# Optimization experiments

Measured on AMD Instinct MI355X. Metric: run time of the kernel, lower is better.

## Reference

```python
import jax, jax.numpy as jnp
import numpy as np

N_NODES = 100000
N_REL = 8
IN_DIM = 64
HID = 128
OUT = 64
N_EDGES = 640000


def setup_inputs() -> dict:
    key = jax.random.key(0)
    ks = jax.random.split(key, 24)

    def w(k, shape, fan_in):
        return jax.random.normal(k, shape, jnp.float32) / np.sqrt(fan_in).astype(np.float32)

    inp = {}
    inp["emb"] = jax.random.normal(ks[0], (N_NODES, IN_DIM), jnp.float32)
    dims = [(IN_DIM, HID), (HID, HID), (HID, HID // 2), (HID // 2, OUT)]
    for i, (di, do) in enumerate(dims, 1):
        inp[f"W{i}"] = w(ks[3 * i], (N_REL, di, do), di)      # per-relation weight
        inp[f"R{i}"] = w(ks[3 * i + 1], (di, do), di)          # root weight
        inp[f"B{i}"] = jnp.zeros((do,), jnp.float32)           # bias
    inp["g1"] = jnp.ones((HID,), jnp.float32)
    inp["b1"] = jnp.zeros((HID,), jnp.float32)
    inp["g2"] = jnp.ones((HID,), jnp.float32)
    inp["b2"] = jnp.zeros((HID,), jnp.float32)
    inp["ei"] = jax.random.randint(ks[20], (2, N_EDGES), 0, N_NODES, jnp.int32)
    inp["et"] = jax.random.randint(ks[21], (N_EDGES,), 0, N_REL, jnp.int32)
    return inp


def rgcn(x, ei, et, W, Wr, b):
    # PyG RGCNConv (aggr='mean'): out_i = x_i @ Wroot + b + sum_r mean_{j in N_r(i)} x_j @ W_r
    # Aggregate-then-transform: mean x[src] per (dst, rel) bin, then per-relation GEMM.
    n, r, d = x.shape[0], W.shape[0], x.shape[1]
    src, dst = ei[0], ei[1]
    seg = dst * r + et                                   # combined (node, relation) segment id
    agg = jax.ops.segment_sum(x[src], seg, num_segments=n * r)          # [N*R, d]
    cnt = jax.ops.segment_sum(jnp.ones((src.shape[0],), x.dtype), seg, num_segments=n * r)
    agg = (agg / jnp.maximum(cnt, 1.0)[:, None]).reshape(n, r, d)       # mean per relation
    return jnp.einsum('nri,rio->no', agg, W) + x @ Wr + b


def layer_norm(x, g, b, eps=1e-5):
    mu = jnp.mean(x, axis=-1, keepdims=True)
    var = jnp.mean((x - mu) ** 2, axis=-1, keepdims=True)
    return (x - mu) * jax.lax.rsqrt(var + eps) * g + b


def reference(emb, W1, R1, B1, W2, R2, B2, W3, R3, B3, W4, R4, B4, g1, b1, g2, b2, ei, et):
    # dropout is eval-mode identity
    x = jax.nn.relu(rgcn(emb, ei, et, W1, R1, B1))
    x = layer_norm(x, g1, b1)
    identity = x
    x = jax.nn.relu(rgcn(x, ei, et, W2, R2, B2))
    x = layer_norm(x + identity, g2, b2)
    x = jax.nn.relu(rgcn(x, ei, et, W3, R3, B3))
    return rgcn(x, ei, et, W4, R4, B4)
```

## Files before the change

kernel.cpp:

```cpp
#include <hip/hip_runtime.h>
#include <math.h>

#define NN 100000
#define NR 8
#define NE 640000
#define SEGN (NN * NR)
#define SPB 2048
#define NSB ((SEGN + SPB - 1) / SPB)

#define TILES 1563
#define HT1 782
#define HT2 781
#define HP1 (HT1 * 64)
#define HP2 (HT2 * 64)
#define HPF (TILES * 64)

typedef __attribute__((ext_vector_type(8))) __bf16 bf16x8;
typedef __attribute__((ext_vector_type(4))) float  f32x4;

__device__ __forceinline__ float bf2f(unsigned short b) {
    return __uint_as_float((unsigned)b << 16);
}
__device__ __forceinline__ unsigned short f2bf(float v) {
    __bf16 b = (__bf16)v;
    return __builtin_bit_cast(unsigned short, b);
}


__global__ __launch_bounds__(256) void count_kernel(
    const int* __restrict__ dst, const int* __restrict__ et, unsigned* __restrict__ cnt) {
    int e = blockIdx.x * 256 + threadIdx.x;
    if (e < NE) atomicAdd(&cnt[(size_t)et[e] * NN + dst[e]], 1u);
}

__global__ __launch_bounds__(256) void scan1_kernel(
    const unsigned* __restrict__ cnt, unsigned* __restrict__ bsum) {
    __shared__ unsigned red[256];
    int b = blockIdx.x, t = threadIdx.x;
    int i0 = b * SPB;
    unsigned s = 0;
#pragma unroll
    for (int k = 0; k < SPB / 256; ++k) {
        int i = i0 + k * 256 + t;
        if (i < SEGN) s += cnt[i];
    }
    red[t] = s;
    __syncthreads();
    for (int off = 128; off >= 1; off >>= 1) {
        if (t < off) red[t] += red[t + off];
        __syncthreads();
    }
    if (t == 0) bsum[b] = red[0];
}

__global__ __launch_bounds__(512) void scan2_kernel(
    unsigned* __restrict__ bsum, int* __restrict__ segoff) {
    __shared__ unsigned buf[512];
    int t = threadIdx.x;
    unsigned v = (t < NSB) ? bsum[t] : 0u;
    buf[t] = v;
    __syncthreads();
    for (int off = 1; off < 512; off <<= 1) {
        unsigned w = (t >= off) ? buf[t - off] : 0u;
        __syncthreads();
        buf[t] += w;
        __syncthreads();
    }
    if (t < NSB) bsum[t] = buf[t] - v;
    if (t == 0) segoff[SEGN] = NE;
}

__global__ __launch_bounds__(256) void scan3_kernel(
    const unsigned* __restrict__ cnt, const unsigned* __restrict__ bsum,
    int* __restrict__ segoff) {
    __shared__ unsigned lc[SPB];
    __shared__ unsigned tsum[256];
    int b = blockIdx.x, t = threadIdx.x;
    int i0 = b * SPB;
#pragma unroll
    for (int k = 0; k < SPB / 256; ++k) {
        int i = i0 + k * 256 + t;
        lc[k * 256 + t] = (i < SEGN) ? cnt[i] : 0u;
    }
    __syncthreads();
    unsigned s = 0;
#pragma unroll
    for (int k = 0; k < 8; ++k) s += lc[t * 8 + k];
    tsum[t] = s;
    __syncthreads();
    for (int off = 1; off < 256; off <<= 1) {
        unsigned w = (t >= off) ? tsum[t - off] : 0u;
        __syncthreads();
        tsum[t] += w;
        __syncthreads();
    }
    unsigned base = bsum[b] + tsum[t] - s;
#pragma unroll
    for (int k = 0; k < 8; ++k) {
        unsigned c = lc[t * 8 + k];
        lc[t * 8 + k] = base;
        base += c;
    }
    __syncthreads();
#pragma unroll
    for (int k = 0; k < SPB / 256; ++k) {
        int i = i0 + k * 256 + t;
        if (i < SEGN) segoff[i] = (int)lc[k * 256 + t];
    }
}

__global__ __launch_bounds__(256) void fill_kernel(
    const int* __restrict__ src, const int* __restrict__ dst, const int* __restrict__ et,
    const int* __restrict__ segoff, unsigned* __restrict__ cursor, int* __restrict__ esrc) {
    int e = blockIdx.x * 256 + threadIdx.x;
    if (e >= NE) return;
    int d = dst[e];
    int seg = et[e] * NN + d;
    int pos = segoff[seg] + (int)atomicAdd(&cursor[seg], 1u);
    esrc[pos] = src[e] | ((d & 3) << 17);
}

__global__ __launch_bounds__(256) void conv_emb(
    const float* __restrict__ emb, ushort* __restrict__ embb) {
    int i = blockIdx.x * 256 + threadIdx.x;
    if (i * 4 >= NN * 64) return;
    f32x4 v = *(const f32x4*)(emb + (size_t)i * 4);
    ushort4 o;
    o.x = f2bf(v[0]); o.y = f2bf(v[1]); o.z = f2bf(v[2]); o.w = f2bf(v[3]);
    *(ushort4*)(embb + (size_t)i * 4) = o;
}


template <int D, int O>
__global__ __launch_bounds__(256) void pack_kernel(
    const float* __restrict__ W, const float* __restrict__ Wr, __bf16* __restrict__ Wp) {
    constexpr int KT = D / 32, NTN = O / 16;
    int idx = blockIdx.x * 256 + threadIdx.x;
    if (idx >= (NR + 1) * KT * NTN * 64) return;
    int l = idx & 63;
    int rest = idx >> 6;
    int nt = rest % NTN; rest /= NTN;
    int kt = rest % KT;
    int r  = rest / KT;
    const float* srcw = (r < NR) ? (W + (size_t)r * D * O) : Wr;
    int n  = nt * 16 + (l & 15);
    int k0 = kt * 32 + (l >> 4) * 8;
    bf16x8 v;
#pragma unroll
    for (int j = 0; j < 8; ++j) {
        int p  = k0 + j;
        int kd = (D == 128) ? ((p >> 1) + ((p & 1) << 6)) : p;
        v[j] = (__bf16)srcw[(size_t)kd * O + n];
    }
    *(bf16x8*)(Wp + (size_t)idx * 8) = v;
}


template <int D, int XF>
__global__ __launch_bounds__(256) void gather_kernel(
    const void* __restrict__ xin, const int* __restrict__ segoff,
    const int* __restrict__ esrc, ushort* __restrict__ agg,
    int nbase, int agg_off, int HP)
{
    int wv = threadIdx.x >> 6, ln = threadIdx.x & 63;
    int r  = blockIdx.y;
    int i0 = blockIdx.x * 16 + wv * 4;
    int n0 = nbase + i0;

    const ushort*   xb = (const ushort*)xin;
    const unsigned* xs = (const unsigned*)xin;

    float ax[4] = {0, 0, 0, 0}, ay[4] = {0, 0, 0, 0};
    int eo[5];
#pragma unroll
    for (int k = 0; k <= 4; ++k) {
        int node = n0 + k; if (node > NN) node = NN;
        eo[k] = segoff[r * NN + node];
    }
    for (int ei = eo[0]; ei < eo[4]; ei += 4) {
        int nb = eo[4] - ei; if (nb > 4) nb = 4;
        int mm[4]; float vx[4], vy[4];
#pragma unroll
        for (int b = 0; b < 4; ++b) mm[b] = (b < nb) ? esrc[ei + b] : 0;
#pragma unroll
        for (int b = 0; b < 4; ++b) {
            if (b < nb) {
                int s = mm[b] & 0x1FFFF;
                if constexpr (XF == 1) {
                    unsigned w = xs[(size_t)s * 64 + ln];
                    vx[b] = bf2f((unsigned short)(w & 0xFFFFu));
                    vy[b] = bf2f((unsigned short)(w >> 16));
                } else {
                    vx[b] = bf2f(xb[(size_t)s * 64 + ln]);
                }
            }
        }
#pragma unroll
        for (int b = 0; b < 4; ++b) {
            if (b < nb) {
                int k = mm[b] >> 17;
#pragma unroll
                for (int kk = 0; kk < 4; ++kk) {
                    ax[kk] += (kk == k) ? vx[b] : 0.0f;
                    if constexpr (D == 128) ay[kk] += (kk == k) ? vy[b] : 0.0f;
                }
            }
        }
    }
#pragma unroll
    for (int k = 0; k < 4; ++k) {
        int c = eo[k + 1] - eo[k];
        float sc = (c > 0) ? 1.0f / (float)c : 0.0f;
        size_t row = ((size_t)r * HP + agg_off + i0 + k) * D;
        if constexpr (D == 128) {
            unsigned st = (unsigned)f2bf(ax[k] * sc) | ((unsigned)f2bf(ay[k] * sc) << 16);
            *((unsigned*)(agg + row) + ln) = st;
        } else {
            agg[row + ln] = f2bf(ax[k] * sc);
        }
    }
}


template <int D, int O, int MODE, int XF, int OF>
__global__ __launch_bounds__(256) void gemm_layer(
    const ushort* __restrict__ agg, const __bf16* __restrict__ Wp,
    const float* __restrict__ bias, const float* __restrict__ gamma,
    const float* __restrict__ beta, const unsigned* __restrict__ xres,
    const void* __restrict__ xroot, void* __restrict__ outv, int base, int HP)
{
    constexpr int KT = D / 32, NTN = O / 16;
    constexpr int PD = (D == 64) ? 8 : 3;
    int tid = threadIdx.x;
    int wv = tid >> 6, ln = tid & 63, lg = ln >> 4, lm = ln & 15;
    int i0 = blockIdx.x * 64 + wv * 16;

    const ushort* abase = agg + ((size_t)(i0 + lm)) * D + lg * 8;

    bf16x8 Aall[NR][KT];
#pragma unroll
    for (int r = 0; r < PD; ++r) {
        const ushort* ar = abase + (size_t)r * HP * D;
#pragma unroll
        for (int kt = 0; kt < KT; ++kt)
            Aall[r][kt] = *(const bf16x8*)(ar + kt * 32);
    }

    bf16x8 Aroot[KT];
    {
        int nrow = base + i0 + lm;
        if (nrow >= NN) nrow = NN - 1;
#pragma unroll
        for (int kt = 0; kt < KT; ++kt) {
            if constexpr (XF == 1) {
                Aroot[kt] = *(const bf16x8*)((const ushort*)xroot +
                                             (size_t)nrow * 128 + kt * 32 + lg * 8);
            } else {
                Aroot[kt] = *(const bf16x8*)((const ushort*)xroot +
                                             (size_t)nrow * 64 + kt * 32 + lg * 8);
            }
        }
    }

    f32x4 acc[NTN];
#pragma unroll
    for (int nt = 0; nt < NTN; ++nt)
#pragma unroll
        for (int q = 0; q < 4; ++q) acc[nt][q] = 0.0f;

#pragma unroll
    for (int r = 0; r < NR; ++r) {
        if (r + PD < NR) {
            const ushort* an = abase + (size_t)(r + PD) * HP * D;
#pragma unroll
            for (int kt = 0; kt < KT; ++kt)
                Aall[r + PD][kt] = *(const bf16x8*)(an + kt * 32);
        }
        const __bf16* bp = Wp + (((size_t)(r * KT) * NTN) << 9) + (ln << 3);
#pragma unroll
        for (int kt = 0; kt < KT; ++kt) {
            const __bf16* bpk = bp + (((size_t)(kt * NTN)) << 9);
#pragma unroll
            for (int nt = 0; nt < NTN; ++nt) {
                bf16x8 B = *(const bf16x8*)(bpk + ((size_t)nt << 9));
                acc[nt] = __builtin_amdgcn_mfma_f32_16x16x32_bf16(Aall[r][kt], B, acc[nt], 0, 0, 0);
            }
        }
    }
    {
        const __bf16* bp = Wp + (((size_t)(8 * KT) * NTN) << 9) + (ln << 3);
#pragma unroll
        for (int kt = 0; kt < KT; ++kt) {
            const __bf16* bpk = bp + (((size_t)(kt * NTN)) << 9);
#pragma unroll
            for (int nt = 0; nt < NTN; ++nt) {
                bf16x8 B = *(const bf16x8*)(bpk + ((size_t)nt << 9));
                acc[nt] = __builtin_amdgcn_mfma_f32_16x16x32_bf16(Aroot[kt], B, acc[nt], 0, 0, 0);
            }
        }
    }

    float bb[NTN], gg[NTN], be[NTN];
#pragma unroll
    for (int nt = 0; nt < NTN; ++nt) {
        bb[nt] = bias[nt * 16 + lm];
        if constexpr (MODE <= 1) {
            gg[nt] = gamma[nt * 16 + lm];
            be[nt] = beta[nt * 16 + lm];
        } else {
            gg[nt] = 0.0f; be[nt] = 0.0f;
        }
    }
#pragma unroll
    for (int q = 0; q < 4; ++q) {
        int row = lg * 4 + q;
        int n = base + i0 + row;
        int nc = (n < NN) ? n : 0;
        float v[NTN];
#pragma unroll
        for (int nt = 0; nt < NTN; ++nt) {
            v[nt] = acc[nt][q] + bb[nt];
            if constexpr (MODE <= 2) v[nt] = fmaxf(v[nt], 0.0f);
            if constexpr (MODE == 1) {
                unsigned w = xres[(size_t)nc * 64 + (nt & 3) * 16 + lm];
                v[nt] += bf2f((unsigned short)((nt < 4) ? (w & 0xFFFFu) : (w >> 16)));
            }
        }
        if constexpr (MODE <= 1) {
            float s1 = 0.0f, s2 = 0.0f;
#pragma unroll
            for (int nt = 0; nt < NTN; ++nt) { s1 += v[nt]; s2 += v[nt] * v[nt]; }
#pragma unroll
            for (int off = 1; off < 16; off <<= 1) {
                s1 += __shfl_xor(s1, off, 64);
                s2 += __shfl_xor(s2, off, 64);
            }
            float mu  = s1 * (1.0f / O);
            float var = s2 * (1.0f / O) - mu * mu;
            float rs  = rsqrtf(var + 1e-5f);
#pragma unroll
            for (int nt = 0; nt < NTN; ++nt) v[nt] = (v[nt] - mu) * rs * gg[nt] + be[nt];
        }
        if (n < NN) {
            if constexpr (OF == 0) {
#pragma unroll
                for (int nt = 0; nt < NTN; ++nt)
                    __builtin_nontemporal_store(
                        v[nt], (float*)outv + (size_t)n * O + nt * 16 + lm);
            } else if constexpr (OF == 1) {
#pragma unroll
                for (int nt = 0; nt < 4; ++nt)
                    ((unsigned*)outv)[(size_t)n * 64 + nt * 16 + lm] =
                        (unsigned)f2bf(v[nt]) | ((unsigned)f2bf(v[nt + 4]) << 16);
            } else {
#pragma unroll
                for (int nt = 0; nt < NTN; ++nt)
                    ((ushort*)outv)[(size_t)n * 64 + nt * 16 + lm] = f2bf(v[nt]);
            }
        }
    }
}


extern "C" void kernel_launch(void* const* d_in, const int* in_sizes, int n_in,
                              void* d_out, int out_size, void* d_ws, size_t ws_size,
                              hipStream_t stream) {
    const float* emb = (const float*)d_in[0];
    const float* W1  = (const float*)d_in[1];
    const float* R1  = (const float*)d_in[2];
    const float* B1  = (const float*)d_in[3];
    const float* W2  = (const float*)d_in[4];
    const float* R2  = (const float*)d_in[5];
    const float* B2  = (const float*)d_in[6];
    const float* W3  = (const float*)d_in[7];
    const float* R3  = (const float*)d_in[8];
    const float* B3  = (const float*)d_in[9];
    const float* W4  = (const float*)d_in[10];
    const float* R4  = (const float*)d_in[11];
    const float* B4  = (const float*)d_in[12];
    const float* g1  = (const float*)d_in[13];
    const float* b1  = (const float*)d_in[14];
    const float* g2  = (const float*)d_in[15];
    const float* b2  = (const float*)d_in[16];
    const int*   ei  = (const int*)d_in[17];
    const int*   et  = (const int*)d_in[18];
    const int* srcp = ei;
    const int* dstp = ei + NE;

    char* ws = (char*)d_ws;
    if (ws_size < 185721872u) return;
    int*      segoff = (int*)(ws + 0);
    int*      esrc   = (int*)(ws + 3200016);
    __bf16*   Wp1    = (__bf16*)(ws + 5760016);
    __bf16*   Wp2    = (__bf16*)(ws + 5907472);
    __bf16*   Wp3    = (__bf16*)(ws + 6202384);
    __bf16*   Wp4    = (__bf16*)(ws + 6349840);
    ushort*   embb   = (ushort*)(ws + 6423568);
    void*     x1     = (void*)(ws + 19223568);
    void*     x2     = (void*)(ws + 44823568);
    void*     x3     = (void*)(ws + 70423568);
    ushort*   agg    = (ushort*)(ws + 83223568);
    unsigned* cnt    = (unsigned*)(ws + 83223568);
    unsigned* cursor = (unsigned*)(ws + 86423568);
    unsigned* bsum   = (unsigned*)(ws + 89623568);
    float*    outp   = (float*)d_out;

    hipMemsetAsync(cnt, 0, 3200000, stream);
    hipMemsetAsync(cursor, 0, 3200000, stream);

    count_kernel<<<(NE + 255) / 256, 256, 0, stream>>>(dstp, et, cnt);
    scan1_kernel<<<NSB, 256, 0, stream>>>(cnt, bsum);
    scan2_kernel<<<1, 512, 0, stream>>>(bsum, segoff);
    scan3_kernel<<<NSB, 256, 0, stream>>>(cnt, bsum, segoff);
    fill_kernel<<<(NE + 255) / 256, 256, 0, stream>>>(
        srcp, dstp, et, segoff, cursor, esrc);
    conv_emb<<<(NN * 64 / 4 + 255) / 256, 256, 0, stream>>>(emb, embb);

    pack_kernel<64, 128><<<(9 * 2 * 8 * 64 + 255) / 256, 256, 0, stream>>>(W1, R1, Wp1);
    pack_kernel<128, 128><<<(9 * 4 * 8 * 64 + 255) / 256, 256, 0, stream>>>(W2, R2, Wp2);
    pack_kernel<128, 64><<<(9 * 4 * 4 * 64 + 255) / 256, 256, 0, stream>>>(W3, R3, Wp3);
    pack_kernel<64, 64><<<(9 * 2 * 4 * 64 + 255) / 256, 256, 0, stream>>>(W4, R4, Wp4);

    gather_kernel<64, 2><<<dim3(HP1 / 16, 8), 256, 0, stream>>>(embb, segoff, esrc, agg, 0, 0, HPF);
    gather_kernel<64, 2><<<dim3(HP2 / 16, 8), 256, 0, stream>>>(embb, segoff, esrc, agg, HP1, HP1, HPF);
    gemm_layer<64, 128, 0, 2, 1><<<HPF / 64, 256, 0, stream>>>(
        agg, Wp1, B1, g1, b1, nullptr, embb, x1, 0, HPF);

    gather_kernel<128, 1><<<dim3(25024 / 16, 8), 256, 0, stream>>>(x1, segoff, esrc, agg, 0, 0, HP1);
    gather_kernel<128, 1><<<dim3(25024 / 16, 8), 256, 0, stream>>>(x1, segoff, esrc, agg, 25024, 25024, HP1);
    gemm_layer<128, 128, 1, 1, 1><<<HP1 / 64, 256, 0, stream>>>(
        agg, Wp2, B2, g2, b2, (const unsigned*)x1, x1, x2, 0, HP1);
    gather_kernel<128, 1><<<dim3(25024 / 16, 8), 256, 0, stream>>>(x1, segoff, esrc, agg, HP1, 0, HP2);
    gather_kernel<128, 1><<<dim3(24960 / 16, 8), 256, 0, stream>>>(x1, segoff, esrc, agg, HP1 + 25024, 25024, HP2);
    gemm_layer<128, 128, 1, 1, 1><<<HP2 / 64, 256, 0, stream>>>(
        agg, Wp2, B2, g2, b2, (const unsigned*)x1, x1, x2, HP1, HP2);

    gather_kernel<128, 1><<<dim3(25024 / 16, 8), 256, 0, stream>>>(x2, segoff, esrc, agg, 0, 0, HP1);
    gather_kernel<128, 1><<<dim3(25024 / 16, 8), 256, 0, stream>>>(x2, segoff, esrc, agg, 25024, 25024, HP1);
    gemm_layer<128, 64, 2, 1, 2><<<HP1 / 64, 256, 0, stream>>>(
        agg, Wp3, B3, nullptr, nullptr, nullptr, x2, x3, 0, HP1);
    gather_kernel<128, 1><<<dim3(25024 / 16, 8), 256, 0, stream>>>(x2, segoff, esrc, agg, HP1, 0, HP2);
    gather_kernel<128, 1><<<dim3(24960 / 16, 8), 256, 0, stream>>>(x2, segoff, esrc, agg, HP1 + 25024, 25024, HP2);
    gemm_layer<128, 64, 2, 1, 2><<<HP2 / 64, 256, 0, stream>>>(
        agg, Wp3, B3, nullptr, nullptr, nullptr, x2, x3, HP1, HP2);

    gather_kernel<64, 2><<<dim3(HP1 / 16, 8), 256, 0, stream>>>(x3, segoff, esrc, agg, 0, 0, HPF);
    gather_kernel<64, 2><<<dim3(HP2 / 16, 8), 256, 0, stream>>>(x3, segoff, esrc, agg, HP1, HP1, HPF);
    gemm_layer<64, 64, 3, 2, 0><<<HPF / 64, 256, 0, stream>>>(
        agg, Wp4, B4, nullptr, nullptr, nullptr, x3, outp, 0, HPF);
}
```

Before: 741.2 us.

## Stage per-relation aggregate tiles through LDS with async global_load_lds double buffering

The GEMM kernel now copies each relation's 64-row aggregate tile into a double-buffered LDS array with global_load_lds, instead of prefetching many relation tiles into registers. The aggregation kernel writes rows with an XOR swizzle so that the LDS reads avoid bank conflicts. The aim is to cut register pressure, which raises occupancy, and to overlap the next relation's load with the current MFMAs. In exchange it adds a __syncthreads per relation and allocates up to 32KB of LDS per block.

```diff
diff --git a/kernel.cpp b/kernel.cpp
--- a/kernel.cpp
+++ b/kernel.cpp
@@ -24,6 +24,12 @@
 __device__ __forceinline__ unsigned short f2bf(float v) {
     __bf16 b = (__bf16)v;
     return __builtin_bit_cast(unsigned short, b);
+}
+
+__device__ __forceinline__ void gload16(const ushort* g, ushort* l) {
+    __builtin_amdgcn_global_load_lds(
+        (const __attribute__((address_space(1))) void*)g,
+        (__attribute__((address_space(3))) void*)l, 16, 0, 0);
 }
 
 
@@ -211,12 +217,13 @@
     for (int k = 0; k < 4; ++k) {
         int c = eo[k + 1] - eo[k];
         float sc = (c > 0) ? 1.0f / (float)c : 0.0f;
-        size_t row = ((size_t)r * HP + agg_off + i0 + k) * D;
+        int rw = agg_off + i0 + k;
+        size_t row = ((size_t)r * HP + rw) * D;
         if constexpr (D == 128) {
             unsigned st = (unsigned)f2bf(ax[k] * sc) | ((unsigned)f2bf(ay[k] * sc) << 16);
-            *((unsigned*)(agg + row) + ln) = st;
+            *((unsigned*)(agg + row) + (ln ^ ((rw & 7) << 2))) = st;
         } else {
-            agg[row + ln] = f2bf(ax[k] * sc);
+            agg[row + (ln ^ ((rw & 7) << 3))] = f2bf(ax[k] * sc);
         }
     }
 }
@@ -230,25 +237,28 @@
     const void* __restrict__ xroot, void* __restrict__ outv, int base, int HP)
 {
     constexpr int KT = D / 32, NTN = O / 16;
-    constexpr int PD = (D == 64) ? 8 : 3;
+    constexpr int NISS = (64 * D * 2) / (4 * 64 * 16);
+    __shared__ __align__(16) ushort sA[2][64 * D];
+
     int tid = threadIdx.x;
     int wv = tid >> 6, ln = tid & 63, lg = ln >> 4, lm = ln & 15;
-    int i0 = blockIdx.x * 64 + wv * 16;
-
-    const ushort* abase = agg + ((size_t)(i0 + lm)) * D + lg * 8;
-
-    bf16x8 Aall[NR][KT];
-#pragma unroll
-    for (int r = 0; r < PD; ++r) {
-        const ushort* ar = abase + (size_t)r * HP * D;
-#pragma unroll
-        for (int kt = 0; kt < KT; ++kt)
-            Aall[r][kt] = *(const bf16x8*)(ar + kt * 32);
-    }
+    int i0 = blockIdx.x * 64;
+
+    auto stage = [&](int r, int b) {
+        const ushort* src = agg + ((size_t)r * HP + i0) * D;
+        ushort* dst = &sA[b][0];
+#pragma unroll
+        for (int j = 0; j < NISS; ++j) {
+            int off_u = wv * (NISS * 512) + j * 512 + ln * 8;
+            gload16(src + off_u, dst + off_u);
+        }
+    };
+
+    stage(0, 0);
 
     bf16x8 Aroot[KT];
     {
-        int nrow = base + i0 + lm;
+        int nrow = base + i0 + wv * 16 + lm;
         if (nrow >= NN) nrow = NN - 1;
 #pragma unroll
         for (int kt = 0; kt < KT; ++kt) {
@@ -268,24 +278,24 @@
 #pragma unroll
         for (int q = 0; q < 4; ++q) acc[nt][q] = 0.0f;
 
-#pragma unroll
+    __syncthreads();
+
+#pragma unroll 1
     for (int r = 0; r < NR; ++r) {
-        if (r + PD < NR) {
-            const ushort* an = abase + (size_t)(r + PD) * HP * D;
-#pragma unroll
-            for (int kt = 0; kt < KT; ++kt)
-                Aall[r + PD][kt] = *(const bf16x8*)(an + kt * 32);
-        }
+        if (r + 1 < NR) stage(r + 1, (r + 1) & 1);
+        const ushort* a_l = &sA[r & 1][(wv * 16 + lm) * D];
         const __bf16* bp = Wp + (((size_t)(r * KT) * NTN) << 9) + (ln << 3);
 #pragma unroll
         for (int kt = 0; kt < KT; ++kt) {
+            bf16x8 A = *(const bf16x8*)(a_l + ((kt * 32 + lg * 8) ^ ((lm & 7) << 3)));
             const __bf16* bpk = bp + (((size_t)(kt * NTN)) << 9);
 #pragma unroll
             for (int nt = 0; nt < NTN; ++nt) {
                 bf16x8 B = *(const bf16x8*)(bpk + ((size_t)nt << 9));
-                acc[nt] = __builtin_amdgcn_mfma_f32_16x16x32_bf16(Aall[r][kt], B, acc[nt], 0, 0, 0);
-            }
-        }
+                acc[nt] = __builtin_amdgcn_mfma_f32_16x16x32_bf16(A, B, acc[nt], 0, 0, 0);
+            }
+        }
+        __syncthreads();
     }
     {
         const __bf16* bp = Wp + (((size_t)(8 * KT) * NTN) << 9) + (ln << 3);
@@ -313,7 +323,7 @@
     }
 #pragma unroll
     for (int q = 0; q < 4; ++q) {
-        int row = lg * 4 + q;
+        int row = wv * 16 + lg * 4 + q;
         int n = base + i0 + row;
         int nc = (n < NN) ? n : 0;
         float v[NTN];
```

New measurement: 786.4 us. 1.06x slower.

## Split GEMM output columns across waves and drop packed row tag in gather

Applied to the files above, without the earlier changes.

The fused GEMM kernel now uses 128-thread blocks. For the 128-wide-input layers, two waves share the same 16 rows and each computes half of the output column tiles, which cuts per-thread accumulator registers and should raise occupancy. LayerNorm statistics for the split case are combined across the two waves through shared memory with a block barrier. Separately, the gather kernel no longer packs the dst&3 tag into esrc. It derives the target row from segment offsets and uses a branch chain instead of predicated adds across all four accumulators. The cost is some redundant A-tile loads across the two waves and an extra barrier.

```diff
diff --git a/kernel.cpp b/kernel.cpp
--- a/kernel.cpp
+++ b/kernel.cpp
@@ -117,7 +117,7 @@
     int d = dst[e];
     int seg = et[e] * NN + d;
     int pos = segoff[seg] + (int)atomicAdd(&cursor[seg], 1u);
-    esrc[pos] = src[e] | ((d & 3) << 17);
+    esrc[pos] = src[e];
 }
 
 __global__ __launch_bounds__(256) void conv_emb(
@@ -177,33 +177,32 @@
         int node = n0 + k; if (node > NN) node = NN;
         eo[k] = segoff[r * NN + node];
     }
-    for (int ei = eo[0]; ei < eo[4]; ei += 4) {
-        int nb = eo[4] - ei; if (nb > 4) nb = 4;
-        int mm[4]; float vx[4], vy[4];
-#pragma unroll
-        for (int b = 0; b < 4; ++b) mm[b] = (b < nb) ? esrc[ei + b] : 0;
+    for (int e4 = eo[0]; e4 < eo[4]; e4 += 4) {
+        int nb = eo[4] - e4; if (nb > 4) nb = 4;
+        int ss[4]; float vx[4], vy[4];
+#pragma unroll
+        for (int b = 0; b < 4; ++b) ss[b] = (b < nb) ? esrc[e4 + b] : 0;
 #pragma unroll
         for (int b = 0; b < 4; ++b) {
             if (b < nb) {
-                int s = mm[b] & 0x1FFFF;
                 if constexpr (XF == 1) {
-                    unsigned w = xs[(size_t)s * 64 + ln];
+                    unsigned w = xs[(size_t)ss[b] * 64 + ln];
                     vx[b] = bf2f((unsigned short)(w & 0xFFFFu));
                     vy[b] = bf2f((unsigned short)(w >> 16));
                 } else {
-                    vx[b] = bf2f(xb[(size_t)s * 64 + ln]);
+                    vx[b] = bf2f(xb[(size_t)ss[b] * 64 + ln]);
                 }
             }
         }
 #pragma unroll
         for (int b = 0; b < 4; ++b) {
             if (b < nb) {
-                int k = mm[b] >> 17;
-#pragma unroll
-                for (int kk = 0; kk < 4; ++kk) {
-                    ax[kk] += (kk == k) ? vx[b] : 0.0f;
-                    if constexpr (D == 128) ay[kk] += (kk == k) ? vy[b] : 0.0f;
-                }
+                int e = e4 + b;
+                int k = (e >= eo[1]) + (e >= eo[2]) + (e >= eo[3]);
+                if (k == 0)      { ax[0] += vx[b]; if constexpr (D == 128) ay[0] += vy[b]; }
+                else if (k == 1) { ax[1] += vx[b]; if constexpr (D == 128) ay[1] += vy[b]; }
+                else if (k == 2) { ax[2] += vx[b]; if constexpr (D == 128) ay[2] += vy[b]; }
+                else             { ax[3] += vx[b]; if constexpr (D == 128) ay[3] += vy[b]; }
             }
         }
     }
@@ -222,18 +221,28 @@
 }
 
 
-template <int D, int O, int MODE, int XF, int OF>
-__global__ __launch_bounds__(256) void gemm_layer(
+template <int D, int O, int MODE, int XF, int OF, int NS>
+__global__ __launch_bounds__(128) void gemm_layer(
     const ushort* __restrict__ agg, const __bf16* __restrict__ Wp,
     const float* __restrict__ bias, const float* __restrict__ gamma,
     const float* __restrict__ beta, const unsigned* __restrict__ xres,
     const void* __restrict__ xroot, void* __restrict__ outv, int base, int HP)
 {
-    constexpr int KT = D / 32, NTN = O / 16;
+    constexpr int KT = D / 32, NTN = O / 16, NTN2 = NTN / NS;
     constexpr int PD = (D == 64) ? 8 : 3;
+    __shared__ float sS[2][4][4], sQ[2][4][4];
+
     int tid = threadIdx.x;
     int wv = tid >> 6, ln = tid & 63, lg = ln >> 4, lm = ln & 15;
-    int i0 = blockIdx.x * 64 + wv * 16;
+    int i0 = (NS == 1) ? (blockIdx.x * 32 + wv * 16) : (blockIdx.x * 16);
+
+    int ng[NTN2];
+#pragma unroll
+    for (int nt = 0; nt < NTN2; ++nt) {
+        if constexpr (NS == 1)       ng[nt] = nt;
+        else if constexpr (O == 128) ng[nt] = wv * 2 + (nt & 1) + (nt >> 1) * 4;
+        else                         ng[nt] = wv * NTN2 + nt;
+    }
 
     const ushort* abase = agg + ((size_t)(i0 + lm)) * D + lg * 8;
 
@@ -262,9 +271,9 @@
         }
     }
 
-    f32x4 acc[NTN];
-#pragma unroll
-    for (int nt = 0; nt < NTN; ++nt)
+    f32x4 acc[NTN2];
+#pragma unroll
+    for (int nt = 0; nt < NTN2; ++nt)
 #pragma unroll
         for (int q = 0; q < 4; ++q) acc[nt][q] = 0.0f;
 
@@ -281,8 +290,8 @@
         for (int kt = 0; kt < KT; ++kt) {
             const __bf16* bpk = bp + (((size_t)(kt * NTN)) << 9);
 #pragma unroll
-            for (int nt = 0; nt < NTN; ++nt) {
-                bf16x8 B = *(const bf16x8*)(bpk + ((size_t)nt << 9));
+            for (int nt = 0; nt < NTN2; ++nt) {
+                bf16x8 B = *(const bf16x8*)(bpk + ((size_t)ng[nt] << 9));
                 acc[nt] = __builtin_amdgcn_mfma_f32_16x16x32_bf16(Aall[r][kt], B, acc[nt], 0, 0, 0);
             }
         }
@@ -293,69 +302,119 @@
         for (int kt = 0; kt < KT; ++kt) {
             const __bf16* bpk = bp + (((size_t)(kt * NTN)) << 9);
 #pragma unroll
-            for (int nt = 0; nt < NTN; ++nt) {
-                bf16x8 B = *(const bf16x8*)(bpk + ((size_t)nt << 9));
+            for (int nt = 0; nt < NTN2; ++nt) {
+                bf16x8 B = *(const bf16x8*)(bpk + ((size_t)ng[nt] << 9));
                 acc[nt] = __builtin_amdgcn_mfma_f32_16x16x32_bf16(Aroot[kt], B, acc[nt], 0, 0, 0);
             }
         }
     }
 
-    float bb[NTN], gg[NTN], be[NTN];
-#pragma unroll
-    for (int nt = 0; nt < NTN; ++nt) {
-        bb[nt] = bias[nt * 16 + lm];
+    float bb[NTN2], gg[NTN2], be[NTN2];
+#pragma unroll
+    for (int nt = 0; nt < NTN2; ++nt) {
+        bb[nt] = bias[ng[nt] * 16 + lm];
         if constexpr (MODE <= 1) {
-            gg[nt] = gamma[nt * 16 + lm];
-            be[nt] = beta[nt * 16 + lm];
+            gg[nt] = gamma[ng[nt] * 16 + lm];
+            be[nt] = beta[ng[nt] * 16 + lm];
         } else {
             gg[nt] = 0.0f; be[nt] = 0.0f;
         }
     }
-#pragma unroll
-    for (int q = 0; q < 4; ++q) {
-        int row = lg * 4 + q;
-        int n = base + i0 + row;
-        int nc = (n < NN) ? n : 0;
-        float v[NTN];
-#pragma unroll
-        for (int nt = 0; nt < NTN; ++nt) {
-            v[nt] = acc[nt][q] + bb[nt];
-            if constexpr (MODE <= 2) v[nt] = fmaxf(v[nt], 0.0f);
-            if constexpr (MODE == 1) {
-                unsigned w = xres[(size_t)nc * 64 + (nt & 3) * 16 + lm];
-                v[nt] += bf2f((unsigned short)((nt < 4) ? (w & 0xFFFFu) : (w >> 16)));
-            }
-        }
-        if constexpr (MODE <= 1) {
+
+    if constexpr (MODE == 1 && NS == 2) {
+        float vv[4][NTN2];
+#pragma unroll
+        for (int q = 0; q < 4; ++q) {
+            int n = base + i0 + lg * 4 + q;
+            int nc = (n < NN) ? n : 0;
+#pragma unroll
+            for (int nt = 0; nt < NTN2; ++nt)
+                vv[q][nt] = fmaxf(acc[nt][q] + bb[nt], 0.0f);
+#pragma unroll
+            for (int nt = 0; nt < 2; ++nt) {
+                unsigned w = xres[(size_t)nc * 64 + (wv * 2 + nt) * 16 + lm];
+                vv[q][nt]     += bf2f((unsigned short)(w & 0xFFFFu));
+                vv[q][nt + 2] += bf2f((unsigned short)(w >> 16));
+            }
+        }
+#pragma unroll
+        for (int q = 0; q < 4; ++q) {
             float s1 = 0.0f, s2 = 0.0f;
 #pragma unroll
-            for (int nt = 0; nt < NTN; ++nt) { s1 += v[nt]; s2 += v[nt] * v[nt]; }
+            for (int nt = 0; nt < NTN2; ++nt) { s1 += vv[q][nt]; s2 += vv[q][nt] * vv[q][nt]; }
 #pragma unroll
             for (int off = 1; off < 16; off <<= 1) {
                 s1 += __shfl_xor(s1, off, 64);
                 s2 += __shfl_xor(s2, off, 64);
             }
+            if (lm == 0) { sS[wv][lg][q] = s1; sQ[wv][lg][q] = s2; }
+        }
+        __syncthreads();
+#pragma unroll
+        for (int q = 0; q < 4; ++q) {
+            int n = base + i0 + lg * 4 + q;
+            float s1 = sS[0][lg][q] + sS[1][lg][q];
+            float s2 = sQ[0][lg][q] + sQ[1][lg][q];
             float mu  = s1 * (1.0f / O);
             float var = s2 * (1.0f / O) - mu * mu;
             float rs  = rsqrtf(var + 1e-5f);
-#pragma unroll
-            for (int nt = 0; nt < NTN; ++nt) v[nt] = (v[nt] - mu) * rs * gg[nt] + be[nt];
-        }
-        if (n < NN) {
-            if constexpr (OF == 0) {
-#pragma unroll
-                for (int nt = 0; nt < NTN; ++nt)
-                    __builtin_nontemporal_store(
-                        v[nt], (float*)outv + (size_t)n * O + nt * 16 + lm);
-            } else if constexpr (OF == 1) {
-#pragma unroll
-                for (int nt = 0; nt < 4; ++nt)
-                    ((unsigned*)outv)[(size_t)n * 64 + nt * 16 + lm] =
-                        (unsigned)f2bf(v[nt]) | ((unsigned)f2bf(v[nt + 4]) << 16);
-            } else {
-#pragma unroll
-                for (int nt = 0; nt < NTN; ++nt)
-                    ((ushort*)outv)[(size_t)n * 64 + nt * 16 + lm] = f2bf(v[nt]);
+            float v[NTN2];
+#pragma unroll
+            for (int nt = 0; nt < NTN2; ++nt) v[nt] = (vv[q][nt] - mu) * rs * gg[nt] + be[nt];
+            if (n < NN) {
+#pragma unroll
+                for (int nt = 0; nt < 2; ++nt)
+                    ((unsigned*)outv)[(size_t)n * 64 + (wv * 2 + nt) * 16 + lm] =
+                        (unsigned)f2bf(v[nt]) | ((unsigned)f2bf(v[nt + 2]) << 16);
+            }
+        }
+    } else {
+#pragma unroll
+        for (int q = 0; q < 4; ++q) {
+            int row = lg * 4 + q;
+            int n = base + i0 + row;
+            int nc = (n < NN) ? n : 0;
+            float v[NTN2];
+#pragma unroll
+            for (int nt = 0; nt < NTN2; ++nt) {
+                v[nt] = acc[nt][q] + bb[nt];
+                if constexpr (MODE <= 2) v[nt] = fmaxf(v[nt], 0.0f);
+                if constexpr (MODE == 1 && NS == 1) {
+                    unsigned w = xres[(size_t)nc * 64 + (nt & 3) * 16 + lm];
+                    v[nt] += bf2f((unsigned short)((nt < 4) ? (w & 0xFFFFu) : (w >> 16)));
+                }
+            }
+            if constexpr (MODE <= 1) {
+                float s1 = 0.0f, s2 = 0.0f;
+#pragma unroll
+                for (int nt = 0; nt < NTN2; ++nt) { s1 += v[nt]; s2 += v[nt] * v[nt]; }
+#pragma unroll
+                for (int off = 1; off < 16; off <<= 1) {
+                    s1 += __shfl_xor(s1, off, 64);
+                    s2 += __shfl_xor(s2, off, 64);
+                }
+                float mu  = s1 * (1.0f / O);
+                float var = s2 * (1.0f / O) - mu * mu;
+                float rs  = rsqrtf(var + 1e-5f);
+#pragma unroll
+                for (int nt = 0; nt < NTN2; ++nt) v[nt] = (v[nt] - mu) * rs * gg[nt] + be[nt];
+            }
+            if (n < NN) {
+                if constexpr (OF == 0) {
+#pragma unroll
+                    for (int nt = 0; nt < NTN2; ++nt)
+                        __builtin_nontemporal_store(
+                            v[nt], (float*)outv + (size_t)n * O + ng[nt] * 16 + lm);
+                } else if constexpr (OF == 1) {
+#pragma unroll
+                    for (int nt = 0; nt < 4; ++nt)
+                        ((unsigned*)outv)[(size_t)n * 64 + nt * 16 + lm] =
+                            (unsigned)f2bf(v[nt]) | ((unsigned)f2bf(v[nt + 4]) << 16);
+                } else {
+#pragma unroll
+                    for (int nt = 0; nt < NTN2; ++nt)
+                        ((ushort*)outv)[(size_t)n * 64 + ng[nt] * 16 + lm] = f2bf(v[nt]);
+                }
             }
         }
     }
@@ -423,29 +482,29 @@
 
     gather_kernel<64, 2><<<dim3(HP1 / 16, 8), 256, 0, stream>>>(embb, segoff, esrc, agg, 0, 0, HPF);
     gather_kernel<64, 2><<<dim3(HP2 / 16, 8), 256, 0, stream>>>(embb, segoff, esrc, agg, HP1, HP1, HPF);
-    gemm_layer<64, 128, 0, 2, 1><<<HPF / 64, 256, 0, stream>>>(
+    gemm_layer<64, 128, 0, 2, 1, 1><<<HPF / 32, 128, 0, stream>>>(
         agg, Wp1, B1, g1, b1, nullptr, embb, x1, 0, HPF);
 
     gather_kernel<128, 1><<<dim3(25024 / 16, 8), 256, 0, stream>>>(x1, segoff, esrc, agg, 0, 0, HP1);
     gather_kernel<128, 1><<<dim3(25024 / 16, 8), 256, 0, stream>>>(x1, segoff, esrc, agg, 25024, 25024, HP1);
-    gemm_layer<128, 128, 1, 1, 1><<<HP1 / 64, 256, 0, stream>>>(
+    gemm_layer<128, 128, 1, 1, 1, 2><<<HP1 / 16, 128, 0, stream>>>(
         agg, Wp2, B2, g2, b2, (const unsigned*)x1, x1, x2, 0, HP1);
     gather_kernel<128, 1><<<dim3(25024 / 16, 8), 256, 0, stream>>>(x1, segoff, esrc, agg, HP1, 0, HP2);
     gather_kernel<128, 1><<<dim3(24960 / 16, 8), 256, 0, stream>>>(x1, segoff, esrc, agg, HP1 + 25024, 25024, HP2);
-    gemm_layer<128, 128, 1, 1, 1><<<HP2 / 64, 256, 0, stream>>>(
+    gemm_layer<128, 128, 1, 1, 1, 2><<<HP2 / 16, 128, 0, stream>>>(
         agg, Wp2, B2, g2, b2, (const unsigned*)x1, x1, x2, HP1, HP2);
 
     gather_kernel<128, 1><<<dim3(25024 / 16, 8), 256, 0, stream>>>(x2, segoff, esrc, agg, 0, 0, HP1);
     gather_kernel<128, 1><<<dim3(25024 / 16, 8), 256, 0, stream>>>(x2, segoff, esrc, agg, 25024, 25024, HP1);
-    gemm_layer<128, 64, 2, 1, 2><<<HP1 / 64, 256, 0, stream>>>(
+    gemm_layer<128, 64, 2, 1, 2, 2><<<HP1 / 16, 128, 0, stream>>>(
         agg, Wp3, B3, nullptr, nullptr, nullptr, x2, x3, 0, HP1);
     gather_kernel<128, 1><<<dim3(25024 / 16, 8), 256, 0, stream>>>(x2, segoff, esrc, agg, HP1, 0, HP2);
     gather_kernel<128, 1><<<dim3(24960 / 16, 8), 256, 0, stream>>>(x2, segoff, esrc, agg, HP1 + 25024, 25024, HP2);
-    gemm_layer<128, 64, 2, 1, 2><<<HP2 / 64, 256, 0, stream>>>(
+    gemm_layer<128, 64, 2, 1, 2, 2><<<HP2 / 16, 128, 0, stream>>>(
         agg, Wp3, B3, nullptr, nullptr, nullptr, x2, x3, HP1, HP2);
 
     gather_kernel<64, 2><<<dim3(HP1 / 16, 8), 256, 0, stream>>>(x3, segoff, esrc, agg, 0, 0, HPF);
     gather_kernel<64, 2><<<dim3(HP2 / 16, 8), 256, 0, stream>>>(x3, segoff, esrc, agg, HP1, HP1, HPF);
-    gemm_layer<64, 64, 3, 2, 0><<<HPF / 64, 256, 0, stream>>>(
+    gemm_layer<64, 64, 3, 2, 0, 1><<<HPF / 32, 128, 0, stream>>>(
         agg, Wp4, B4, nullptr, nullptr, nullptr, x3, outp, 0, HPF);
 }
```

After: 847.8 us. +14.4%, slower.
